# Performance work log

Hardware: AMD Instinct MI355X
Metric: run time of the kernel (lower is better)

Reference implementation:

```python
import jax, jax.numpy as jnp
import numpy as np

E, B, S, C, N, D, DFF, H, K_FREQ = 4, 16, 256, 17, 16, 32, 64, 4, 4
DH = D // H
MA_KERNELS = (4, 8, 12)


def setup_inputs() -> dict:
    key = jax.random.key(0)
    ks = jax.random.split(key, 16)
    sc = 1.0 / np.sqrt(D).astype(np.float32)
    inp = {
        "x": jax.random.normal(ks[0], (B, S, C, 1), jnp.float32),
        "original_x": jax.random.uniform(ks[1], (B, S, 2), jnp.float32),
        "start_W": jax.random.normal(ks[2], (D,), jnp.float32),
        "start_b": jnp.zeros((D,), jnp.float32),
        "Wq": jax.random.normal(ks[3], (E, D, D), jnp.float32) * sc,
        "Wk": jax.random.normal(ks[4], (E, D, D), jnp.float32) * sc,
        "Wv": jax.random.normal(ks[5], (E, D, D), jnp.float32) * sc,
        "Wo": jax.random.normal(ks[6], (E, D, D), jnp.float32) * sc,
        "ln1_g": jnp.ones((E, D), jnp.float32),
        "ln1_b": jnp.zeros((E, D), jnp.float32),
        "ln2_g": jnp.ones((E, D), jnp.float32),
        "ln2_b": jnp.zeros((E, D), jnp.float32),
        "W1": jax.random.normal(ks[7], (E, D, DFF), jnp.float32) * sc,
        "b1": jnp.zeros((E, DFF), jnp.float32),
        "W2": jax.random.normal(ks[8], (E, DFF, D), jnp.float32) * (1.0 / np.sqrt(DFF).astype(np.float32)),
        "b2": jnp.zeros((E, D), jnp.float32),
    }
    return inp


def _moving_avg(x, k):
    # x: [B,S,Ch], replicate-pad then uniform window of size k (stride 1)
    front = jnp.repeat(x[:, :1], (k - 1) // 2, axis=1)
    end = jnp.repeat(x[:, -1:], k // 2, axis=1)
    xp = jnp.concatenate([front, x, end], axis=1)  # [B, S+k-1, Ch]
    c = jnp.cumsum(xp, axis=1)
    c = jnp.concatenate([jnp.zeros_like(c[:, :1]), c], axis=1)
    return (c[:, k:] - c[:, :-k]) / jnp.asarray(k, x.dtype)


def _fourier_season(x, k):
    # ETSformer-style FourierLayer: keep top-k amplitude frequencies (excluding DC)
    s = x.shape[1]
    xf = jnp.fft.rfft(x, axis=1)            # [B,F,Ch] complex
    amp = jnp.abs(xf)
    amp = amp.at[:, 0, :].set(-jnp.inf)     # exclude DC
    topv = jax.lax.top_k(jnp.moveaxis(amp, 1, -1), k)[0]  # [B,Ch,k]
    thresh = topv[..., -1]                  # [B,Ch]
    mask = amp >= thresh[:, None, :]
    xf_m = jnp.where(mask, xf, 0)
    return jnp.fft.irfft(xf_m, n=s, axis=1).astype(x.dtype)


def _ln(z, g, b):
    m = jnp.mean(z, -1, keepdims=True)
    v = jnp.var(z, -1, keepdims=True)
    return (z - m) * jax.lax.rsqrt(v + 1e-5) * g + b


def _expert_fwd(args):
    h, wq, wk, wv, wo, g1, bg1, g2, bg2, w1, b1e, w2, b2e = args
    # h: [B,S,N,D]; pre-LN MHA over the sequence axis per (batch, node)
    z = _ln(h, g1, bg1)
    q = jnp.einsum('bsnd,de->bsne', z, wq).reshape(B, S, N, H, DH)
    k_ = jnp.einsum('bsnd,de->bsne', z, wk).reshape(B, S, N, H, DH)
    v_ = jnp.einsum('bsnd,de->bsne', z, wv).reshape(B, S, N, H, DH)
    att = jnp.einsum('bqnhd,bknhd->bnhqk', q, k_) * (1.0 / np.sqrt(DH).astype(np.float32))
    att = jax.nn.softmax(att, axis=-1)
    o = jnp.einsum('bnhqk,bknhd->bqnhd', att, v_).reshape(B, S, N, D)
    h = h + jnp.einsum('bsnd,de->bsne', o, wo)
    z2 = _ln(h, g2, bg2)
    f = jax.nn.relu(jnp.einsum('bsnd,df->bsnf', z2, w1) + b1e)
    h = h + jnp.einsum('bsnf,fd->bsnd', f, w2) + b2e
    return h


def reference(x, original_x, start_W, start_b, Wq, Wk, Wv, Wo,
              ln1_g, ln1_b, ln2_g, ln2_b, W1, b1, W2, b2):
    xc = x[:, :, :, 0]                                  # [B,S,C]
    trend = sum(_moving_avg(xc, k) for k in MA_KERNELS) / float(len(MA_KERNELS))
    season = _fourier_season(xc, K_FREQ)
    new_x = xc + season + trend                         # [B,S,C]

    scores = original_x[:, :, -1]                       # [B,S]
    bins = jnp.linspace(scores.min(), scores.max(), E + 1)
    assign = jnp.clip(jnp.searchsorted(bins, scores, side='right') - 1, 0, E - 1)  # [B,S] int

    xns = new_x[:, :, :-1]                              # [B,S,N] drop score channel
    onehot = (assign[None] == jnp.arange(E)[:, None, None])          # [E,B,S] bool
    expert_in = xns[None] * onehot[..., None].astype(xns.dtype)      # [E,B,S,N] dense zero-padded dispatch
    hidden = expert_in[..., None] * start_W + start_b                # [E,B,S,N,D] start_linear

    outs = jax.lax.map(_expert_fwd, (hidden, Wq, Wk, Wv, Wo,
                                     ln1_g, ln1_b, ln2_g, ln2_b, W1, b1, W2, b2))  # [E,B,S,N,D]
    combined = jnp.einsum('ebs,ebsnd->bsnd', onehot.astype(outs.dtype), outs)      # one-hot combine
    return combined
```

## Files before the change

### kernel.cpp

```cpp
#include <hip/hip_runtime.h>
#include <hip/hip_fp16.h>
#include <math.h>

#define BB 16
#define SS 256
#define CC 17
#define NCH 16
#define DD 32
#define DFFN 64
#define HH 4
#define DH 8
#define EE 4

#define WS_K0 16
#define WS_V0 144
#define WS_XNS 512
#define WS_SPI (WS_XNS + BB*SS*NCH)
#define WS_WT  (WS_SPI + BB*SS + 64)
#define WS_WL  (WS_WT + 6144)

#define PRE 0.51006977f

typedef __fp16 hv2 __attribute__((ext_vector_type(2)));

__device__ __forceinline__ unsigned pkh2(float a, float b) {
  hv2 r = __builtin_amdgcn_cvt_pkrtz(a, b);
  unsigned u; __builtin_memcpy(&u, &r, 4);
  return u;
}
__device__ __forceinline__ float fd2(unsigned a, unsigned b, float c) {
  hv2 av, bv;
  __builtin_memcpy(&av, &a, 4);
  __builtin_memcpy(&bv, &b, 4);
  return __builtin_amdgcn_fdot2(av, bv, c, false);
}
__device__ __forceinline__ __half2 u2h2(unsigned u) {
  __half2 h; __builtin_memcpy(&h, &u, 4); return h;
}
template<int PAT>
__device__ __forceinline__ unsigned qdpp(unsigned v) {
  return (unsigned)__builtin_amdgcn_mov_dpp((int)v, PAT, 0xF, 0xF, true);
}
template<int PAT>
__device__ __forceinline__ float qdppf(float v) {
  return __uint_as_float(qdpp<PAT>(__float_as_uint(v)));
}

__launch_bounds__(1024)
__global__ void decomp_prep_kernel(const float* __restrict__ x,
                                   const float* __restrict__ ox,
                                   const float* __restrict__ sb,
                                   const float* __restrict__ g1,
                                   const float* __restrict__ bb1,
                                   const float* __restrict__ Wq,
                                   const float* __restrict__ Wk,
                                   const float* __restrict__ Wv,
                                   const float* __restrict__ Wo,
                                   const float* __restrict__ W1,
                                   const float* __restrict__ W2,
                                   float* __restrict__ ws) {
  const int t = threadIdx.x;
  if (blockIdx.x < 256) {
    const int b = blockIdx.x / NCH;
    const int c = blockIdx.x % NCH;
    __shared__ float xs[SS];
    __shared__ float prr[1024], pii[1024];
    __shared__ float amp[129];
    __shared__ float2 YY[129];
    __shared__ float sth;
    if (t < SS) xs[t] = x[(b*SS + t)*CC + c];
    __syncthreads();
    const float TH0 = 0.024543692606170259f;
    {
      const int f = (t & 127) + 1;
      const int chunk = t >> 7;
      const int s0 = chunk * 32;
      const int ph0 = (f * s0) & 255;
      float si, cr; sincosf(TH0*(float)ph0, &si, &cr);
      float s1, c1; sincosf(TH0*(float)f, &s1, &c1);
      float xr = 0.f, xi = 0.f;
      #pragma unroll 4
      for (int k = 0; k < 32; ++k) {
        float xvv = xs[s0 + k];
        xr += xvv * cr;
        xi -= xvv * si;
        float nc = cr*c1 - si*s1;
        si = si*c1 + cr*s1;
        cr = nc;
      }
      prr[t] = xr; pii[t] = xi;
    }
    __syncthreads();
    if (t < 128) {
      float xr = 0.f, xi = 0.f;
      #pragma unroll
      for (int k2 = 0; k2 < 8; ++k2) { xr += prr[t + 128*k2]; xi += pii[t + 128*k2]; }
      prr[t] = xr; pii[t] = xi;
      amp[t+1] = sqrtf(xr*xr + xi*xi);
    }
    __syncthreads();
    if (t < 64) {
      float a0 = amp[t+1], a1 = amp[t+65];
      int i0 = t+1, i1 = t+65;
      float th = -1e30f;
      for (int r = 0; r < 4; ++r) {
        float mv = (a0 > a1) ? a0 : a1;
        int   mi = (a0 > a1) ? i0 : i1;
        for (int off = 32; off > 0; off >>= 1) {
          float ov = __shfl_xor(mv, off);
          int   oi = __shfl_xor(mi, off);
          if (ov > mv || (ov == mv && oi < mi)) { mv = ov; mi = oi; }
        }
        th = mv;
        if (mi == i0) a0 = -1e30f;
        if (mi == i1) a1 = -1e30f;
      }
      if (t == 0) sth = th;
    }
    __syncthreads();
    if (t < 128) {
      const int f = t + 1;
      float wgt = (amp[f] >= sth) ? ((f == 128) ? 1.0f : 2.0f) * (1.0f/256.0f) : 0.0f;
      YY[f] = make_float2(wgt * prr[t], wgt * pii[t]);
    }
    __syncthreads();
    {
      const int s = t & 255;
      const int fc = t >> 8;
      const int f0 = 1 + fc*32;
      const int ph0 = (s * f0) & 255;
      float si, cr; sincosf(TH0*(float)ph0, &si, &cr);
      float s1, c1; sincosf(TH0*(float)s, &s1, &c1);
      float acc = 0.f;
      #pragma unroll 4
      for (int k = 0; k < 32; ++k) {
        float2 y = YY[f0 + k];
        acc += y.x*cr - y.y*si;
        float nc = cr*c1 - si*s1;
        si = si*c1 + cr*s1;
        cr = nc;
      }
      prr[t] = acc;
    }
    __syncthreads();
    if (t < 256) {
      float season = prr[t] + prr[t+256] + prr[t+512] + prr[t+768];
      float s4 = 0.f, s8 = 0.f, s12 = 0.f;
      #pragma unroll
      for (int j = 0; j < 4; ++j)  { int p = t + j - 1; p = p < 0 ? 0 : (p > SS-1 ? SS-1 : p); s4  += xs[p]; }
      #pragma unroll
      for (int j = 0; j < 8; ++j)  { int p = t + j - 3; p = p < 0 ? 0 : (p > SS-1 ? SS-1 : p); s8  += xs[p]; }
      #pragma unroll
      for (int j = 0; j < 12; ++j) { int p = t + j - 5; p = p < 0 ? 0 : (p > SS-1 ? SS-1 : p); s12 += xs[p]; }
      float trend = (s4 * 0.25f + s8 * 0.125f + s12 * (1.0f/12.0f)) * (1.0f/3.0f);
      ws[WS_XNS + (b*SS + t)*NCH + c] = xs[t] + season + trend;
    }
  } else if (blockIdx.x < 272) {
    const int b = blockIdx.x - 256;
    __shared__ float red[32];
    __shared__ int asg[SS];
    __shared__ int cnt[EE];
    __shared__ float z0[EE*DD];
    float mn = 3e38f, mx = -3e38f;
    #pragma unroll
    for (int k = 0; k < 4; ++k) {
      float v = ox[(t + k*1024)*2 + 1];
      mn = fminf(mn, v); mx = fmaxf(mx, v);
    }
    for (int off = 32; off > 0; off >>= 1) {
      mn = fminf(mn, __shfl_xor(mn, off));
      mx = fmaxf(mx, __shfl_xor(mx, off));
    }
    if ((t & 63) == 0) { red[(t>>6)*2] = mn; red[(t>>6)*2+1] = mx; }
    __syncthreads();
    mn = red[0]; mx = red[1];
    #pragma unroll
    for (int w = 1; w < 16; ++w) { mn = fminf(mn, red[w*2]); mx = fmaxf(mx, red[w*2+1]); }
    const float step = (mx - mn) * 0.25f;
    const float e1 = mn + step, e2 = mn + 2.f*step, e3 = mn + 3.f*step;
    if (t < 256) {
      float sc = ox[(b*SS + t)*2 + 1];
      asg[t] = (sc >= e1) + (sc >= e2) + (sc >= e3);
    }
    __syncthreads();
    if (t < EE) {
      int c = 0;
      for (int s2 = 0; s2 < SS; ++s2) c += (asg[s2] == t);
      cnt[t] = c;
    }
    __syncthreads();
    int* SPw  = (int*)ws + WS_SPI;
    int* OFFw = SPw + BB*SS;
    if (t < EE) {
      int off = 0;
      for (int i = 0; i < t; ++i) off += cnt[i];
      OFFw[b*EE + t] = off;
      int kp = off;
      for (int s2 = 0; s2 < SS; ++s2) if (asg[s2] == t) SPw[b*SS + (kp++)] = s2;
    }
    if (t < 128) {
      int ee = t >> 5, d = t & 31;
      float m = 0.f;
      for (int i = 0; i < DD; ++i) m += sb[i];
      m *= (1.0f/DD);
      float var = 0.f;
      for (int i = 0; i < DD; ++i) { float df = sb[i]-m; var += df*df; }
      var *= (1.0f/DD);
      float rs = rsqrtf(var + 1e-5f);
      z0[ee*DD + d] = (sb[d]-m)*rs*g1[ee*DD+d] + bb1[ee*DD+d];
    }
    __syncthreads();
    if (b == 0 && t < 128) {
      int ee = t >> 5, d = t & 31;
      float k0 = 0.f, v0 = 0.f;
      for (int i = 0; i < DD; ++i) {
        float zz = z0[ee*DD + i];
        k0 += zz * Wk[ee*DD*DD + i*DD + d];
        v0 += zz * Wv[ee*DD*DD + i*DD + d];
      }
      ws[WS_K0 + ee*DD + d] = k0;
      ws[WS_V0 + ee*DD + d] = v0;
    }
  } else {
    unsigned* img = (unsigned*)ws + WS_WT;
    const int base_u = (blockIdx.x - 272)*4096;
    #pragma unroll
    for (int i = 0; i < 4; ++i) {
      int u = base_u + i*1024 + t;
      unsigned val;
      if (u < 6144) {
        int mat = u >> 11, r = u & 2047;
        int row = r >> 4, ip = r & 15;
        int e = row >> 5, q = row & 31;
        int d = (q & 3)*8 + (q >> 2);
        const float* Wm = (mat == 0) ? Wq : (mat == 1) ? Wk : Wv;
        const float* src = Wm + e*1024 + d;
        val = pkh2(src[ip*64], src[ip*64 + 32]);
      } else {
        int v = u - 6144;
        if (v < 2048) {
          int row = v >> 4, ip = v & 15;
          int e = row >> 5, q = row & 31;
          int d = (q & 3)*8 + (q >> 2);
          const float* src = Wo + e*1024 + d;
          val = pkh2(src[ip*64], src[ip*64 + 32]);
        } else if (v < 6144) {
          int r = v - 2048;
          int row = r >> 4, ip = r & 15;
          int e = row >> 6, q = row & 63;
          int j = (q & 3)*16 + (q >> 2);
          const float* src = W1 + e*2048 + j;
          val = pkh2(src[ip*128], src[ip*128 + 64]);
        } else {
          int r = v - 6144;
          int a = r >> 11, rr = r & 2047;
          int row = rr >> 4, ip = rr & 15;
          int e = row >> 5, q = row & 31;
          int d = (q & 3)*8 + (q >> 2);
          int jp = a*16 + ip;
          const float* src = W2 + e*2048 + d;
          val = pkh2(src[2*jp*32], src[(2*jp+1)*32]);
        }
      }
      img[u] = val;
    }
  }
}

__launch_bounds__(1024, 4)
__global__ void fused_kernel(const float* __restrict__ ws,
    const float* __restrict__ g1, const float* __restrict__ bb1,
    const float* __restrict__ sW, const float* __restrict__ sb,
    const float* __restrict__ g2, const float* __restrict__ bb2,
    const float* __restrict__ b1, const float* __restrict__ b2,
    float* __restrict__ out) {
  const int blk = blockIdx.x;
  const int n = blk & 15;
  const int b = blk >> 4;
  const int t = threadIdx.x;
  const int p = t >> 2;
  const int hh = t & 3;
  __shared__ unsigned lds[24576];
  unsigned* wT = lds + 8192;
  unsigned* wl = lds + 14336;

  {
    const unsigned* img = (const unsigned*)ws + WS_WT;
    const int wv = t >> 6;
    const int ln = t & 63;
    #pragma unroll
    for (int i = 0; i < 4; ++i) {
      const int ch = wv*4 + i;
      __builtin_amdgcn_global_load_lds(
          (const __attribute__((address_space(1))) unsigned*)(img + ch*256 + ln*4),
          (__attribute__((address_space(3))) unsigned*)(wT + ch*256 + ln*4),
          16, 0, 0);
    }
  }

  const int* SP  = (const int*)ws + WS_SPI;
  const int* OFF = SP + BB*SS;
  const int o1 = OFF[b*4+1], o2v = OFF[b*4+2], o3 = OFF[b*4+3];
  const int e = (p >= o1) + (p >= o2v) + (p >= o3);
  const int beg = (e==0) ? 0  : ((e==1) ? o1 : ((e==2) ? o2v : o3));
  const int end = (e==0) ? o1 : ((e==1) ? o2v : ((e==2) ? o3 : SS));
  const int s = SP[b*SS + p];
  const float xv = ws[WS_XNS + (b*SS + s)*NCH + n];

  float h[DD];
  #pragma unroll
  for (int d = 0; d < DD; ++d) h[d] = xv * sW[d] + sb[d];
  float m = 0.f;
  #pragma unroll
  for (int d = 0; d < DD; ++d) m += h[d];
  m *= (1.0f/DD);
  float var = 0.f;
  #pragma unroll
  for (int d = 0; d < DD; ++d) { float df = h[d]-m; var += df*df; }
  var *= (1.0f/DD);
  float rs = rsqrtf(var + 1e-5f);
  unsigned zp[16];
  #pragma unroll
  for (int ip = 0; ip < 16; ++ip) {
    float za = (h[2*ip]  -m)*rs*g1[e*DD+2*ip]   + bb1[e*DD+2*ip];
    float zb = (h[2*ip+1]-m)*rs*g1[e*DD+2*ip+1] + bb1[e*DD+2*ip+1];
    zp[ip] = pkh2(za, zb);
  }
  __syncthreads();

  float q[DH], kk[DH], vv[DH];
  #pragma unroll
  for (int dd = 0; dd < DH; ++dd) {
    const int row16 = (e*32 + dd*4 + hh)*16;
    const uint4* rq = (const uint4*)&wT[row16];
    const uint4* rk = (const uint4*)&wT[2048 + row16];
    const uint4* rv = (const uint4*)&wT[4096 + row16];
    float aq = 0.f, ak = 0.f, av = 0.f;
    #pragma unroll
    for (int g4 = 0; g4 < 4; ++g4) {
      uint4 wq4 = rq[g4], wk4 = rk[g4], wv4 = rv[g4];
      aq = fd2(zp[4*g4+0], wq4.x, aq); aq = fd2(zp[4*g4+1], wq4.y, aq);
      aq = fd2(zp[4*g4+2], wq4.z, aq); aq = fd2(zp[4*g4+3], wq4.w, aq);
      ak = fd2(zp[4*g4+0], wk4.x, ak); ak = fd2(zp[4*g4+1], wk4.y, ak);
      ak = fd2(zp[4*g4+2], wk4.z, ak); ak = fd2(zp[4*g4+3], wk4.w, ak);
      av = fd2(zp[4*g4+0], wv4.x, av); av = fd2(zp[4*g4+1], wv4.y, av);
      av = fd2(zp[4*g4+2], wv4.z, av); av = fd2(zp[4*g4+3], wv4.w, av);
    }
    q[dd] = aq * PRE; kk[dd] = ak; vv[dd] = av;
  }
  *(uint4*)&lds[p*32 + hh*8]     = make_uint4(pkh2(kk[0],kk[1]), pkh2(kk[2],kk[3]),
                                              pkh2(kk[4],kk[5]), pkh2(kk[6],kk[7]));
  *(uint4*)&lds[p*32 + hh*8 + 4] = make_uint4(pkh2(vv[0],vv[1]), pkh2(vv[2],vv[3]),
                                              pkh2(vv[4],vv[5]), pkh2(vv[6],vv[7]));
  unsigned qp2[4];
  #pragma unroll
  for (int i = 0; i < 4; ++i) qp2[i] = pkh2(q[2*i], q[2*i+1]);
  float s0 = 0.f;
  #pragma unroll
  for (int d = 0; d < DH; ++d) s0 += q[d] * ws[WS_K0 + e*DD + hh*DH + d];
  __syncthreads();

  float wsum = 0.f;
  __half2 o2[4];
  #pragma unroll
  for (int i = 0; i < 4; ++i) o2[i] = u2h2(0u);
  int jk = beg;
  for (; jk + 1 < end; jk += 2) {
    uint4 ku0 = *(const uint4*)&lds[jk*32 + hh*8];
    uint4 vu0 = *(const uint4*)&lds[jk*32 + hh*8 + 4];
    uint4 ku1 = *(const uint4*)&lds[(jk+1)*32 + hh*8];
    uint4 vu1 = *(const uint4*)&lds[(jk+1)*32 + hh*8 + 4];
    float a0 = 0.f, a1 = 0.f;
    a0 = fd2(qp2[0], ku0.x, a0); a0 = fd2(qp2[1], ku0.y, a0);
    a0 = fd2(qp2[2], ku0.z, a0); a0 = fd2(qp2[3], ku0.w, a0);
    a1 = fd2(qp2[0], ku1.x, a1); a1 = fd2(qp2[1], ku1.y, a1);
    a1 = fd2(qp2[2], ku1.z, a1); a1 = fd2(qp2[3], ku1.w, a1);
    float w0f = __builtin_amdgcn_exp2f(a0);
    float w1f = __builtin_amdgcn_exp2f(a1);
    wsum += w0f + w1f;
    __half2 w20 = u2h2(pkh2(w0f, w0f));
    __half2 w21 = u2h2(pkh2(w1f, w1f));
    o2[0] = __hfma2(w20, u2h2(vu0.x), o2[0]);
    o2[1] = __hfma2(w20, u2h2(vu0.y), o2[1]);
    o2[2] = __hfma2(w20, u2h2(vu0.z), o2[2]);
    o2[3] = __hfma2(w20, u2h2(vu0.w), o2[3]);
    o2[0] = __hfma2(w21, u2h2(vu1.x), o2[0]);
    o2[1] = __hfma2(w21, u2h2(vu1.y), o2[1]);
    o2[2] = __hfma2(w21, u2h2(vu1.z), o2[2]);
    o2[3] = __hfma2(w21, u2h2(vu1.w), o2[3]);
  }
  if (jk < end) {
    uint4 ku = *(const uint4*)&lds[jk*32 + hh*8];
    uint4 vu = *(const uint4*)&lds[jk*32 + hh*8 + 4];
    float a = 0.f;
    a = fd2(qp2[0], ku.x, a); a = fd2(qp2[1], ku.y, a);
    a = fd2(qp2[2], ku.z, a); a = fd2(qp2[3], ku.w, a);
    float wf = __builtin_amdgcn_exp2f(a);
    wsum += wf;
    __half2 w2 = u2h2(pkh2(wf, wf));
    o2[0] = __hfma2(w2, u2h2(vu.x), o2[0]);
    o2[1] = __hfma2(w2, u2h2(vu.y), o2[1]);
    o2[2] = __hfma2(w2, u2h2(vu.z), o2[2]);
    o2[3] = __hfma2(w2, u2h2(vu.w), o2[3]);
  }
  float o[DH];
  #pragma unroll
  for (int i = 0; i < 4; ++i) {
    o[2*i]   = __low2float(o2[i]);
    o[2*i+1] = __high2float(o2[i]);
  }
  const int nmis = SS - (end - beg);
  float w0 = (float)nmis * __builtin_amdgcn_exp2f(s0);
  wsum += w0;
  #pragma unroll
  for (int d = 0; d < DH; ++d) o[d] += w0 * ws[WS_V0 + e*DD + hh*DH + d];
  float inv = 1.0f / wsum;
  #pragma unroll
  for (int d = 0; d < DH; ++d) o[d] *= inv;

  unsigned oq[4];
  #pragma unroll
  for (int j = 0; j < 4; ++j) oq[j] = pkh2(o[2*j], o[2*j+1]);
  unsigned ovp[16];
  #pragma unroll
  for (int j = 0; j < 4; ++j) {
    ovp[j]    = qdpp<0x00>(oq[j]);
    ovp[4+j]  = qdpp<0x55>(oq[j]);
    ovp[8+j]  = qdpp<0xAA>(oq[j]);
    ovp[12+j] = qdpp<0xFF>(oq[j]);
  }

  float acc[DH];
  #pragma unroll
  for (int dd = 0; dd < DH; ++dd) {
    int d = hh*DH + dd;
    const uint4* row = (const uint4*)&wl[(e*32 + dd*4 + hh)*16];
    float a = xv * sW[d] + sb[d];
    #pragma unroll
    for (int g4 = 0; g4 < 4; ++g4) {
      uint4 w4 = row[g4];
      a = fd2(ovp[4*g4+0], w4.x, a); a = fd2(ovp[4*g4+1], w4.y, a);
      a = fd2(ovp[4*g4+2], w4.z, a); a = fd2(ovp[4*g4+3], w4.w, a);
    }
    acc[dd] = a;
  }

  float ssum = 0.f;
  #pragma unroll
  for (int dd = 0; dd < DH; ++dd) ssum += acc[dd];
  ssum += qdppf<0xB1>(ssum);
  ssum += qdppf<0x4E>(ssum);
  float m2 = ssum * (1.0f/DD);
  float vs = 0.f;
  #pragma unroll
  for (int dd = 0; dd < DH; ++dd) { float df = acc[dd]-m2; vs += df*df; }
  vs += qdppf<0xB1>(vs);
  vs += qdppf<0x4E>(vs);
  float rs2 = rsqrtf(vs * (1.0f/DD) + 1e-5f);
  unsigned zq[4];
  #pragma unroll
  for (int j = 0; j < 4; ++j) {
    int d = hh*DH + 2*j;
    float za = (acc[2*j]  -m2)*rs2*g2[e*DD+d]   + bb2[e*DD+d];
    float zb = (acc[2*j+1]-m2)*rs2*g2[e*DD+d+1] + bb2[e*DD+d+1];
    zq[j] = pkh2(za, zb);
  }
  unsigned zp2[16];
  #pragma unroll
  for (int j = 0; j < 4; ++j) {
    zp2[j]    = qdpp<0x00>(zq[j]);
    zp2[4+j]  = qdpp<0x55>(zq[j]);
    zp2[8+j]  = qdpp<0xAA>(zq[j]);
    zp2[12+j] = qdpp<0xFF>(zq[j]);
  }

  float f[16];
  #pragma unroll
  for (int jj = 0; jj < 16; ++jj) {
    const uint4* row = (const uint4*)&wl[2048 + (e*64 + jj*4 + hh)*16];
    float a = b1[e*DFFN + hh*16 + jj];
    #pragma unroll
    for (int g4 = 0; g4 < 4; ++g4) {
      uint4 w4 = row[g4];
      a = fd2(zp2[4*g4+0], w4.x, a); a = fd2(zp2[4*g4+1], w4.y, a);
      a = fd2(zp2[4*g4+2], w4.z, a); a = fd2(zp2[4*g4+3], w4.w, a);
    }
    f[jj] = fmaxf(a, 0.0f);
  }
  unsigned fq[8];
  #pragma unroll
  for (int j = 0; j < 8; ++j) fq[j] = pkh2(f[2*j], f[2*j+1]);
  unsigned fu[32];
  #pragma unroll
  for (int j = 0; j < 8; ++j) {
    fu[j]    = qdpp<0x00>(fq[j]);
    fu[8+j]  = qdpp<0x55>(fq[j]);
    fu[16+j] = qdpp<0xAA>(fq[j]);
    fu[24+j] = qdpp<0xFF>(fq[j]);
  }

  float acc2[DH];
  #pragma unroll
  for (int dd = 0; dd < DH; ++dd) {
    int d = hh*DH + dd;
    const int row16 = (e*32 + dd*4 + hh)*16;
    float a = acc[dd] + b2[e*DD + d];
    #pragma unroll
    for (int g4 = 0; g4 < 8; ++g4) {
      const int plane = (g4 >> 2);
      uint4 w4 = *(const uint4*)&wl[6144 + plane*2048 + row16 + 4*(g4 & 3)];
      a = fd2(fu[4*g4+0], w4.x, a); a = fd2(fu[4*g4+1], w4.y, a);
      a = fd2(fu[4*g4+2], w4.z, a); a = fd2(fu[4*g4+3], w4.w, a);
    }
    acc2[dd] = a;
  }
  float* op = out + ((size_t)((b*SS + s)*NCH + n))*DD + hh*DH;
  *(float4*)(op)     = make_float4(acc2[0], acc2[1], acc2[2], acc2[3]);
  *(float4*)(op + 4) = make_float4(acc2[4], acc2[5], acc2[6], acc2[7]);
}

extern "C" void kernel_launch(void* const* d_in, const int* in_sizes, int n_in,
                              void* d_out, int out_size, void* d_ws, size_t ws_size,
                              hipStream_t stream) {
  (void)in_sizes; (void)n_in; (void)out_size; (void)ws_size;
  const float* x   = (const float*)d_in[0];
  const float* ox  = (const float*)d_in[1];
  const float* sW  = (const float*)d_in[2];
  const float* sb  = (const float*)d_in[3];
  const float* Wq  = (const float*)d_in[4];
  const float* Wk  = (const float*)d_in[5];
  const float* Wv  = (const float*)d_in[6];
  const float* Wo  = (const float*)d_in[7];
  const float* g1  = (const float*)d_in[8];
  const float* b1n = (const float*)d_in[9];
  const float* g2  = (const float*)d_in[10];
  const float* b2n = (const float*)d_in[11];
  const float* W1  = (const float*)d_in[12];
  const float* bf1 = (const float*)d_in[13];
  const float* W2  = (const float*)d_in[14];
  const float* bf2 = (const float*)d_in[15];
  float* out = (float*)d_out;
  float* ws  = (float*)d_ws;

  decomp_prep_kernel<<<276, 1024, 0, stream>>>(x, ox, sb, g1, b1n,
                                               Wq, Wk, Wv, Wo, W1, W2, ws);
  fused_kernel<<<BB*NCH, 1024, 0, stream>>>(ws, g1, b1n, sW, sb, g2, b2n,
                                            bf1, bf2, out);
}
```

Before: 134.4 us.

## Process two query positions per thread to reuse K/V and weight loads

Each thread now handles two adjacent sorted positions, halving the block size to 512 threads. The attention loop reads each K/V row once from LDS and applies it to both queries, masking each by its expert range. Weight rows are shared when both positions map to the same expert. This roughly doubles register pressure and adds masked exp work in the attention loop, in exchange for fewer LDS loads and a smaller block.

```diff
diff --git a/kernel.cpp b/kernel.cpp
--- a/kernel.cpp
+++ b/kernel.cpp
@@ -267,7 +267,7 @@
   }
 }
 
-__launch_bounds__(1024, 4)
+__launch_bounds__(512, 2)
 __global__ void fused_kernel(const float* __restrict__ ws,
     const float* __restrict__ g1, const float* __restrict__ bb1,
     const float* __restrict__ sW, const float* __restrict__ sb,
@@ -278,8 +278,9 @@
   const int n = blk & 15;
   const int b = blk >> 4;
   const int t = threadIdx.x;
-  const int p = t >> 2;
+  const int pp = t >> 2;
   const int hh = t & 3;
+  const int p0 = pp*2, p1 = pp*2 + 1;
   __shared__ unsigned lds[24576];
   unsigned* wT = lds + 8192;
   unsigned* wl = lds + 14336;
@@ -289,8 +290,8 @@
     const int wv = t >> 6;
     const int ln = t & 63;
     #pragma unroll
-    for (int i = 0; i < 4; ++i) {
-      const int ch = wv*4 + i;
+    for (int i = 0; i < 8; ++i) {
+      const int ch = wv*8 + i;
       __builtin_amdgcn_global_load_lds(
           (const __attribute__((address_space(1))) unsigned*)(img + ch*256 + ln*4),
           (__attribute__((address_space(3))) unsigned*)(wT + ch*256 + ln*4),
@@ -301,222 +302,339 @@
   const int* SP  = (const int*)ws + WS_SPI;
   const int* OFF = SP + BB*SS;
   const int o1 = OFF[b*4+1], o2v = OFF[b*4+2], o3 = OFF[b*4+3];
-  const int e = (p >= o1) + (p >= o2v) + (p >= o3);
-  const int beg = (e==0) ? 0  : ((e==1) ? o1 : ((e==2) ? o2v : o3));
-  const int end = (e==0) ? o1 : ((e==1) ? o2v : ((e==2) ? o3 : SS));
-  const int s = SP[b*SS + p];
-  const float xv = ws[WS_XNS + (b*SS + s)*NCH + n];
-
-  float h[DD];
-  #pragma unroll
-  for (int d = 0; d < DD; ++d) h[d] = xv * sW[d] + sb[d];
-  float m = 0.f;
-  #pragma unroll
-  for (int d = 0; d < DD; ++d) m += h[d];
-  m *= (1.0f/DD);
-  float var = 0.f;
-  #pragma unroll
-  for (int d = 0; d < DD; ++d) { float df = h[d]-m; var += df*df; }
-  var *= (1.0f/DD);
-  float rs = rsqrtf(var + 1e-5f);
-  unsigned zp[16];
-  #pragma unroll
-  for (int ip = 0; ip < 16; ++ip) {
-    float za = (h[2*ip]  -m)*rs*g1[e*DD+2*ip]   + bb1[e*DD+2*ip];
-    float zb = (h[2*ip+1]-m)*rs*g1[e*DD+2*ip+1] + bb1[e*DD+2*ip+1];
-    zp[ip] = pkh2(za, zb);
+  const int e0 = (p0 >= o1) + (p0 >= o2v) + (p0 >= o3);
+  const int e1 = (p1 >= o1) + (p1 >= o2v) + (p1 >= o3);
+  const bool same_e = (e0 == e1);
+  const int beg0 = (e0==0) ? 0  : ((e0==1) ? o1 : ((e0==2) ? o2v : o3));
+  const int end0 = (e0==0) ? o1 : ((e0==1) ? o2v : ((e0==2) ? o3 : SS));
+  const int beg1 = (e1==0) ? 0  : ((e1==1) ? o1 : ((e1==2) ? o2v : o3));
+  const int end1 = (e1==0) ? o1 : ((e1==1) ? o2v : ((e1==2) ? o3 : SS));
+  const int sA = SP[b*SS + p0];
+  const int sB = SP[b*SS + p1];
+  const float xv0 = ws[WS_XNS + (b*SS + sA)*NCH + n];
+  const float xv1 = ws[WS_XNS + (b*SS + sB)*NCH + n];
+
+  unsigned zp0[16], zp1[16];
+  {
+    float h[DD];
+    #pragma unroll
+    for (int d = 0; d < DD; ++d) h[d] = xv0 * sW[d] + sb[d];
+    float m = 0.f;
+    #pragma unroll
+    for (int d = 0; d < DD; ++d) m += h[d];
+    m *= (1.0f/DD);
+    float var = 0.f;
+    #pragma unroll
+    for (int d = 0; d < DD; ++d) { float df = h[d]-m; var += df*df; }
+    float rs = rsqrtf(var*(1.0f/DD) + 1e-5f);
+    #pragma unroll
+    for (int ip = 0; ip < 16; ++ip) {
+      float za = (h[2*ip]  -m)*rs*g1[e0*DD+2*ip]   + bb1[e0*DD+2*ip];
+      float zb = (h[2*ip+1]-m)*rs*g1[e0*DD+2*ip+1] + bb1[e0*DD+2*ip+1];
+      zp0[ip] = pkh2(za, zb);
+    }
+  }
+  {
+    float h[DD];
+    #pragma unroll
+    for (int d = 0; d < DD; ++d) h[d] = xv1 * sW[d] + sb[d];
+    float m = 0.f;
+    #pragma unroll
+    for (int d = 0; d < DD; ++d) m += h[d];
+    m *= (1.0f/DD);
+    float var = 0.f;
+    #pragma unroll
+    for (int d = 0; d < DD; ++d) { float df = h[d]-m; var += df*df; }
+    float rs = rsqrtf(var*(1.0f/DD) + 1e-5f);
+    #pragma unroll
+    for (int ip = 0; ip < 16; ++ip) {
+      float za = (h[2*ip]  -m)*rs*g1[e1*DD+2*ip]   + bb1[e1*DD+2*ip];
+      float zb = (h[2*ip+1]-m)*rs*g1[e1*DD+2*ip+1] + bb1[e1*DD+2*ip+1];
+      zp1[ip] = pkh2(za, zb);
+    }
   }
   __syncthreads();
 
-  float q[DH], kk[DH], vv[DH];
+  float q0[DH], q1[DH], kk0[DH], kk1[DH], vv0[DH], vv1[DH];
   #pragma unroll
   for (int dd = 0; dd < DH; ++dd) {
-    const int row16 = (e*32 + dd*4 + hh)*16;
-    const uint4* rq = (const uint4*)&wT[row16];
-    const uint4* rk = (const uint4*)&wT[2048 + row16];
-    const uint4* rv = (const uint4*)&wT[4096 + row16];
-    float aq = 0.f, ak = 0.f, av = 0.f;
+    const int r0 = (e0*32 + dd*4 + hh)*16;
+    const uint4* rq = (const uint4*)&wT[r0];
+    const uint4* rk = (const uint4*)&wT[2048 + r0];
+    const uint4* rv = (const uint4*)&wT[4096 + r0];
+    float aq0=0.f, ak0=0.f, av0=0.f, aq1=0.f, ak1=0.f, av1=0.f;
     #pragma unroll
     for (int g4 = 0; g4 < 4; ++g4) {
       uint4 wq4 = rq[g4], wk4 = rk[g4], wv4 = rv[g4];
-      aq = fd2(zp[4*g4+0], wq4.x, aq); aq = fd2(zp[4*g4+1], wq4.y, aq);
-      aq = fd2(zp[4*g4+2], wq4.z, aq); aq = fd2(zp[4*g4+3], wq4.w, aq);
-      ak = fd2(zp[4*g4+0], wk4.x, ak); ak = fd2(zp[4*g4+1], wk4.y, ak);
-      ak = fd2(zp[4*g4+2], wk4.z, ak); ak = fd2(zp[4*g4+3], wk4.w, ak);
-      av = fd2(zp[4*g4+0], wv4.x, av); av = fd2(zp[4*g4+1], wv4.y, av);
-      av = fd2(zp[4*g4+2], wv4.z, av); av = fd2(zp[4*g4+3], wv4.w, av);
-    }
-    q[dd] = aq * PRE; kk[dd] = ak; vv[dd] = av;
-  }
-  *(uint4*)&lds[p*32 + hh*8]     = make_uint4(pkh2(kk[0],kk[1]), pkh2(kk[2],kk[3]),
-                                              pkh2(kk[4],kk[5]), pkh2(kk[6],kk[7]));
-  *(uint4*)&lds[p*32 + hh*8 + 4] = make_uint4(pkh2(vv[0],vv[1]), pkh2(vv[2],vv[3]),
-                                              pkh2(vv[4],vv[5]), pkh2(vv[6],vv[7]));
-  unsigned qp2[4];
-  #pragma unroll
-  for (int i = 0; i < 4; ++i) qp2[i] = pkh2(q[2*i], q[2*i+1]);
-  float s0 = 0.f;
-  #pragma unroll
-  for (int d = 0; d < DH; ++d) s0 += q[d] * ws[WS_K0 + e*DD + hh*DH + d];
+      aq0 = fd2(zp0[4*g4+0], wq4.x, aq0); aq0 = fd2(zp0[4*g4+1], wq4.y, aq0);
+      aq0 = fd2(zp0[4*g4+2], wq4.z, aq0); aq0 = fd2(zp0[4*g4+3], wq4.w, aq0);
+      ak0 = fd2(zp0[4*g4+0], wk4.x, ak0); ak0 = fd2(zp0[4*g4+1], wk4.y, ak0);
+      ak0 = fd2(zp0[4*g4+2], wk4.z, ak0); ak0 = fd2(zp0[4*g4+3], wk4.w, ak0);
+      av0 = fd2(zp0[4*g4+0], wv4.x, av0); av0 = fd2(zp0[4*g4+1], wv4.y, av0);
+      av0 = fd2(zp0[4*g4+2], wv4.z, av0); av0 = fd2(zp0[4*g4+3], wv4.w, av0);
+      if (same_e) {
+        aq1 = fd2(zp1[4*g4+0], wq4.x, aq1); aq1 = fd2(zp1[4*g4+1], wq4.y, aq1);
+        aq1 = fd2(zp1[4*g4+2], wq4.z, aq1); aq1 = fd2(zp1[4*g4+3], wq4.w, aq1);
+        ak1 = fd2(zp1[4*g4+0], wk4.x, ak1); ak1 = fd2(zp1[4*g4+1], wk4.y, ak1);
+        ak1 = fd2(zp1[4*g4+2], wk4.z, ak1); ak1 = fd2(zp1[4*g4+3], wk4.w, ak1);
+        av1 = fd2(zp1[4*g4+0], wv4.x, av1); av1 = fd2(zp1[4*g4+1], wv4.y, av1);
+        av1 = fd2(zp1[4*g4+2], wv4.z, av1); av1 = fd2(zp1[4*g4+3], wv4.w, av1);
+      }
+    }
+    if (!same_e) {
+      const int r1 = (e1*32 + dd*4 + hh)*16;
+      const uint4* rq1p = (const uint4*)&wT[r1];
+      const uint4* rk1p = (const uint4*)&wT[2048 + r1];
+      const uint4* rv1p = (const uint4*)&wT[4096 + r1];
+      #pragma unroll
+      for (int g4 = 0; g4 < 4; ++g4) {
+        uint4 wq4 = rq1p[g4], wk4 = rk1p[g4], wv4 = rv1p[g4];
+        aq1 = fd2(zp1[4*g4+0], wq4.x, aq1); aq1 = fd2(zp1[4*g4+1], wq4.y, aq1);
+        aq1 = fd2(zp1[4*g4+2], wq4.z, aq1); aq1 = fd2(zp1[4*g4+3], wq4.w, aq1);
+        ak1 = fd2(zp1[4*g4+0], wk4.x, ak1); ak1 = fd2(zp1[4*g4+1], wk4.y, ak1);
+        ak1 = fd2(zp1[4*g4+2], wk4.z, ak1); ak1 = fd2(zp1[4*g4+3], wk4.w, ak1);
+        av1 = fd2(zp1[4*g4+0], wv4.x, av1); av1 = fd2(zp1[4*g4+1], wv4.y, av1);
+        av1 = fd2(zp1[4*g4+2], wv4.z, av1); av1 = fd2(zp1[4*g4+3], wv4.w, av1);
+      }
+    }
+    q0[dd] = aq0 * PRE; kk0[dd] = ak0; vv0[dd] = av0;
+    q1[dd] = aq1 * PRE; kk1[dd] = ak1; vv1[dd] = av1;
+  }
+  *(uint4*)&lds[p0*32 + hh*8]     = make_uint4(pkh2(kk0[0],kk0[1]), pkh2(kk0[2],kk0[3]),
+                                               pkh2(kk0[4],kk0[5]), pkh2(kk0[6],kk0[7]));
+  *(uint4*)&lds[p0*32 + hh*8 + 4] = make_uint4(pkh2(vv0[0],vv0[1]), pkh2(vv0[2],vv0[3]),
+                                               pkh2(vv0[4],vv0[5]), pkh2(vv0[6],vv0[7]));
+  *(uint4*)&lds[p1*32 + hh*8]     = make_uint4(pkh2(kk1[0],kk1[1]), pkh2(kk1[2],kk1[3]),
+                                               pkh2(kk1[4],kk1[5]), pkh2(kk1[6],kk1[7]));
+  *(uint4*)&lds[p1*32 + hh*8 + 4] = make_uint4(pkh2(vv1[0],vv1[1]), pkh2(vv1[2],vv1[3]),
+                                               pkh2(vv1[4],vv1[5]), pkh2(vv1[6],vv1[7]));
+  unsigned qp20[4], qp21[4];
+  #pragma unroll
+  for (int i = 0; i < 4; ++i) {
+    qp20[i] = pkh2(q0[2*i], q0[2*i+1]);
+    qp21[i] = pkh2(q1[2*i], q1[2*i+1]);
+  }
+  float sc0 = 0.f, sc1 = 0.f;
+  #pragma unroll
+  for (int d = 0; d < DH; ++d) {
+    sc0 += q0[d] * ws[WS_K0 + e0*DD + hh*DH + d];
+    sc1 += q1[d] * ws[WS_K0 + e1*DD + hh*DH + d];
+  }
   __syncthreads();
 
-  float wsum = 0.f;
-  __half2 o2[4];
-  #pragma unroll
-  for (int i = 0; i < 4; ++i) o2[i] = u2h2(0u);
-  int jk = beg;
-  for (; jk + 1 < end; jk += 2) {
-    uint4 ku0 = *(const uint4*)&lds[jk*32 + hh*8];
-    uint4 vu0 = *(const uint4*)&lds[jk*32 + hh*8 + 4];
-    uint4 ku1 = *(const uint4*)&lds[(jk+1)*32 + hh*8];
-    uint4 vu1 = *(const uint4*)&lds[(jk+1)*32 + hh*8 + 4];
+  float wsum0 = 0.f, wsum1 = 0.f;
+  __half2 oa[4], ob[4];
+  #pragma unroll
+  for (int i = 0; i < 4; ++i) { oa[i] = u2h2(0u); ob[i] = u2h2(0u); }
+  for (int j = beg0; j < end1; ++j) {
+    uint4 ku = *(const uint4*)&lds[j*32 + hh*8];
+    uint4 vu = *(const uint4*)&lds[j*32 + hh*8 + 4];
     float a0 = 0.f, a1 = 0.f;
-    a0 = fd2(qp2[0], ku0.x, a0); a0 = fd2(qp2[1], ku0.y, a0);
-    a0 = fd2(qp2[2], ku0.z, a0); a0 = fd2(qp2[3], ku0.w, a0);
-    a1 = fd2(qp2[0], ku1.x, a1); a1 = fd2(qp2[1], ku1.y, a1);
-    a1 = fd2(qp2[2], ku1.z, a1); a1 = fd2(qp2[3], ku1.w, a1);
-    float w0f = __builtin_amdgcn_exp2f(a0);
-    float w1f = __builtin_amdgcn_exp2f(a1);
-    wsum += w0f + w1f;
-    __half2 w20 = u2h2(pkh2(w0f, w0f));
-    __half2 w21 = u2h2(pkh2(w1f, w1f));
-    o2[0] = __hfma2(w20, u2h2(vu0.x), o2[0]);
-    o2[1] = __hfma2(w20, u2h2(vu0.y), o2[1]);
-    o2[2] = __hfma2(w20, u2h2(vu0.z), o2[2]);
-    o2[3] = __hfma2(w20, u2h2(vu0.w), o2[3]);
-    o2[0] = __hfma2(w21, u2h2(vu1.x), o2[0]);
-    o2[1] = __hfma2(w21, u2h2(vu1.y), o2[1]);
-    o2[2] = __hfma2(w21, u2h2(vu1.z), o2[2]);
-    o2[3] = __hfma2(w21, u2h2(vu1.w), o2[3]);
-  }
-  if (jk < end) {
-    uint4 ku = *(const uint4*)&lds[jk*32 + hh*8];
-    uint4 vu = *(const uint4*)&lds[jk*32 + hh*8 + 4];
-    float a = 0.f;
-    a = fd2(qp2[0], ku.x, a); a = fd2(qp2[1], ku.y, a);
-    a = fd2(qp2[2], ku.z, a); a = fd2(qp2[3], ku.w, a);
-    float wf = __builtin_amdgcn_exp2f(a);
-    wsum += wf;
-    __half2 w2 = u2h2(pkh2(wf, wf));
-    o2[0] = __hfma2(w2, u2h2(vu.x), o2[0]);
-    o2[1] = __hfma2(w2, u2h2(vu.y), o2[1]);
-    o2[2] = __hfma2(w2, u2h2(vu.z), o2[2]);
-    o2[3] = __hfma2(w2, u2h2(vu.w), o2[3]);
-  }
-  float o[DH];
+    a0 = fd2(qp20[0], ku.x, a0); a0 = fd2(qp20[1], ku.y, a0);
+    a0 = fd2(qp20[2], ku.z, a0); a0 = fd2(qp20[3], ku.w, a0);
+    a1 = fd2(qp21[0], ku.x, a1); a1 = fd2(qp21[1], ku.y, a1);
+    a1 = fd2(qp21[2], ku.z, a1); a1 = fd2(qp21[3], ku.w, a1);
+    float w0k = (j < end0)  ? __builtin_amdgcn_exp2f(a0) : 0.f;
+    float w1k = (j >= beg1) ? __builtin_amdgcn_exp2f(a1) : 0.f;
+    wsum0 += w0k; wsum1 += w1k;
+    __half2 w20 = u2h2(pkh2(w0k, w0k));
+    __half2 w21 = u2h2(pkh2(w1k, w1k));
+    oa[0] = __hfma2(w20, u2h2(vu.x), oa[0]);
+    oa[1] = __hfma2(w20, u2h2(vu.y), oa[1]);
+    oa[2] = __hfma2(w20, u2h2(vu.z), oa[2]);
+    oa[3] = __hfma2(w20, u2h2(vu.w), oa[3]);
+    ob[0] = __hfma2(w21, u2h2(vu.x), ob[0]);
+    ob[1] = __hfma2(w21, u2h2(vu.y), ob[1]);
+    ob[2] = __hfma2(w21, u2h2(vu.z), ob[2]);
+    ob[3] = __hfma2(w21, u2h2(vu.w), ob[3]);
+  }
+  float o0[DH], o1v[DH];
   #pragma unroll
   for (int i = 0; i < 4; ++i) {
-    o[2*i]   = __low2float(o2[i]);
-    o[2*i+1] = __high2float(o2[i]);
-  }
-  const int nmis = SS - (end - beg);
-  float w0 = (float)nmis * __builtin_amdgcn_exp2f(s0);
-  wsum += w0;
-  #pragma unroll
-  for (int d = 0; d < DH; ++d) o[d] += w0 * ws[WS_V0 + e*DD + hh*DH + d];
-  float inv = 1.0f / wsum;
-  #pragma unroll
-  for (int d = 0; d < DH; ++d) o[d] *= inv;
-
-  unsigned oq[4];
-  #pragma unroll
-  for (int j = 0; j < 4; ++j) oq[j] = pkh2(o[2*j], o[2*j+1]);
-  unsigned ovp[16];
-  #pragma unroll
-  for (int j = 0; j < 4; ++j) {
-    ovp[j]    = qdpp<0x00>(oq[j]);
-    ovp[4+j]  = qdpp<0x55>(oq[j]);
-    ovp[8+j]  = qdpp<0xAA>(oq[j]);
-    ovp[12+j] = qdpp<0xFF>(oq[j]);
-  }
-
-  float acc[DH];
+    o0[2*i]   = __low2float(oa[i]);  o0[2*i+1]  = __high2float(oa[i]);
+    o1v[2*i]  = __low2float(ob[i]);  o1v[2*i+1] = __high2float(ob[i]);
+  }
+  {
+    const int nm0 = SS - (end0 - beg0);
+    const int nm1 = SS - (end1 - beg1);
+    float w00 = (float)nm0 * __builtin_amdgcn_exp2f(sc0);
+    float w01 = (float)nm1 * __builtin_amdgcn_exp2f(sc1);
+    wsum0 += w00; wsum1 += w01;
+    #pragma unroll
+    for (int d = 0; d < DH; ++d) {
+      o0[d]  += w00 * ws[WS_V0 + e0*DD + hh*DH + d];
+      o1v[d] += w01 * ws[WS_V0 + e1*DD + hh*DH + d];
+    }
+    float i0 = 1.0f / wsum0, i1 = 1.0f / wsum1;
+    #pragma unroll
+    for (int d = 0; d < DH; ++d) { o0[d] *= i0; o1v[d] *= i1; }
+  }
+
+  unsigned ovp0[16], ovp1[16];
+  {
+    unsigned oqa[4], oqb[4];
+    #pragma unroll
+    for (int j = 0; j < 4; ++j) {
+      oqa[j] = pkh2(o0[2*j], o0[2*j+1]);
+      oqb[j] = pkh2(o1v[2*j], o1v[2*j+1]);
+    }
+    #pragma unroll
+    for (int j = 0; j < 4; ++j) {
+      ovp0[j]    = qdpp<0x00>(oqa[j]);  ovp1[j]    = qdpp<0x00>(oqb[j]);
+      ovp0[4+j]  = qdpp<0x55>(oqa[j]);  ovp1[4+j]  = qdpp<0x55>(oqb[j]);
+      ovp0[8+j]  = qdpp<0xAA>(oqa[j]);  ovp1[8+j]  = qdpp<0xAA>(oqb[j]);
+      ovp0[12+j] = qdpp<0xFF>(oqa[j]);  ovp1[12+j] = qdpp<0xFF>(oqb[j]);
+    }
+  }
+
+  float acc0[DH], acc1[DH];
   #pragma unroll
   for (int dd = 0; dd < DH; ++dd) {
-    int d = hh*DH + dd;
-    const uint4* row = (const uint4*)&wl[(e*32 + dd*4 + hh)*16];
-    float a = xv * sW[d] + sb[d];
+    const int d = hh*DH + dd;
+    const uint4* row0 = (const uint4*)&wl[(e0*32 + dd*4 + hh)*16];
+    float a0 = xv0 * sW[d] + sb[d];
+    float a1 = xv1 * sW[d] + sb[d];
     #pragma unroll
     for (int g4 = 0; g4 < 4; ++g4) {
-      uint4 w4 = row[g4];
-      a = fd2(ovp[4*g4+0], w4.x, a); a = fd2(ovp[4*g4+1], w4.y, a);
-      a = fd2(ovp[4*g4+2], w4.z, a); a = fd2(ovp[4*g4+3], w4.w, a);
-    }
-    acc[dd] = a;
-  }
-
-  float ssum = 0.f;
-  #pragma unroll
-  for (int dd = 0; dd < DH; ++dd) ssum += acc[dd];
-  ssum += qdppf<0xB1>(ssum);
-  ssum += qdppf<0x4E>(ssum);
-  float m2 = ssum * (1.0f/DD);
-  float vs = 0.f;
-  #pragma unroll
-  for (int dd = 0; dd < DH; ++dd) { float df = acc[dd]-m2; vs += df*df; }
-  vs += qdppf<0xB1>(vs);
-  vs += qdppf<0x4E>(vs);
-  float rs2 = rsqrtf(vs * (1.0f/DD) + 1e-5f);
-  unsigned zq[4];
-  #pragma unroll
-  for (int j = 0; j < 4; ++j) {
-    int d = hh*DH + 2*j;
-    float za = (acc[2*j]  -m2)*rs2*g2[e*DD+d]   + bb2[e*DD+d];
-    float zb = (acc[2*j+1]-m2)*rs2*g2[e*DD+d+1] + bb2[e*DD+d+1];
-    zq[j] = pkh2(za, zb);
-  }
-  unsigned zp2[16];
-  #pragma unroll
-  for (int j = 0; j < 4; ++j) {
-    zp2[j]    = qdpp<0x00>(zq[j]);
-    zp2[4+j]  = qdpp<0x55>(zq[j]);
-    zp2[8+j]  = qdpp<0xAA>(zq[j]);
-    zp2[12+j] = qdpp<0xFF>(zq[j]);
-  }
-
-  float f[16];
+      uint4 w4 = row0[g4];
+      a0 = fd2(ovp0[4*g4+0], w4.x, a0); a0 = fd2(ovp0[4*g4+1], w4.y, a0);
+      a0 = fd2(ovp0[4*g4+2], w4.z, a0); a0 = fd2(ovp0[4*g4+3], w4.w, a0);
+      if (same_e) {
+        a1 = fd2(ovp1[4*g4+0], w4.x, a1); a1 = fd2(ovp1[4*g4+1], w4.y, a1);
+        a1 = fd2(ovp1[4*g4+2], w4.z, a1); a1 = fd2(ovp1[4*g4+3], w4.w, a1);
+      }
+    }
+    if (!same_e) {
+      const uint4* row1 = (const uint4*)&wl[(e1*32 + dd*4 + hh)*16];
+      #pragma unroll
+      for (int g4 = 0; g4 < 4; ++g4) {
+        uint4 w4 = row1[g4];
+        a1 = fd2(ovp1[4*g4+0], w4.x, a1); a1 = fd2(ovp1[4*g4+1], w4.y, a1);
+        a1 = fd2(ovp1[4*g4+2], w4.z, a1); a1 = fd2(ovp1[4*g4+3], w4.w, a1);
+      }
+    }
+    acc0[dd] = a0; acc1[dd] = a1;
+  }
+
+  unsigned zq20[16], zq21[16];
+  {
+    float s0s = 0.f, s1s = 0.f;
+    #pragma unroll
+    for (int dd = 0; dd < DH; ++dd) { s0s += acc0[dd]; s1s += acc1[dd]; }
+    s0s += qdppf<0xB1>(s0s); s0s += qdppf<0x4E>(s0s);
+    s1s += qdppf<0xB1>(s1s); s1s += qdppf<0x4E>(s1s);
+    float m0 = s0s * (1.0f/DD), m1 = s1s * (1.0f/DD);
+    float v0 = 0.f, v1 = 0.f;
+    #pragma unroll
+    for (int dd = 0; dd < DH; ++dd) {
+      float d0 = acc0[dd]-m0; v0 += d0*d0;
+      float d1 = acc1[dd]-m1; v1 += d1*d1;
+    }
+    v0 += qdppf<0xB1>(v0); v0 += qdppf<0x4E>(v0);
+    v1 += qdppf<0xB1>(v1); v1 += qdppf<0x4E>(v1);
+    float r0 = rsqrtf(v0*(1.0f/DD) + 1e-5f);
+    float r1 = rsqrtf(v1*(1.0f/DD) + 1e-5f);
+    unsigned za0[4], za1[4];
+    #pragma unroll
+    for (int j = 0; j < 4; ++j) {
+      int d = hh*DH + 2*j;
+      float x0 = (acc0[2*j]  -m0)*r0*g2[e0*DD+d]   + bb2[e0*DD+d];
+      float y0 = (acc0[2*j+1]-m0)*r0*g2[e0*DD+d+1] + bb2[e0*DD+d+1];
+      float x1 = (acc1[2*j]  -m1)*r1*g2[e1*DD+d]   + bb2[e1*DD+d];
+      float y1 = (acc1[2*j+1]-m1)*r1*g2[e1*DD+d+1] + bb2[e1*DD+d+1];
+      za0[j] = pkh2(x0, y0);
+      za1[j] = pkh2(x1, y1);
+    }
+    #pragma unroll
+    for (int j = 0; j < 4; ++j) {
+      zq20[j]    = qdpp<0x00>(za0[j]);  zq21[j]    = qdpp<0x00>(za1[j]);
+      zq20[4+j]  = qdpp<0x55>(za0[j]);  zq21[4+j]  = qdpp<0x55>(za1[j]);
+      zq20[8+j]  = qdpp<0xAA>(za0[j]);  zq21[8+j]  = qdpp<0xAA>(za1[j]);
+      zq20[12+j] = qdpp<0xFF>(za0[j]);  zq21[12+j] = qdpp<0xFF>(za1[j]);
+    }
+  }
+
+  float f0[16], f1[16];
   #pragma unroll
   for (int jj = 0; jj < 16; ++jj) {
-    const uint4* row = (const uint4*)&wl[2048 + (e*64 + jj*4 + hh)*16];
-    float a = b1[e*DFFN + hh*16 + jj];
+    const uint4* row0 = (const uint4*)&wl[2048 + (e0*64 + jj*4 + hh)*16];
+    float a0 = b1[e0*DFFN + hh*16 + jj];
+    float a1 = b1[e1*DFFN + hh*16 + jj];
     #pragma unroll
     for (int g4 = 0; g4 < 4; ++g4) {
-      uint4 w4 = row[g4];
-      a = fd2(zp2[4*g4+0], w4.x, a); a = fd2(zp2[4*g4+1], w4.y, a);
-      a = fd2(zp2[4*g4+2], w4.z, a); a = fd2(zp2[4*g4+3], w4.w, a);
-    }
-    f[jj] = fmaxf(a, 0.0f);
-  }
-  unsigned fq[8];
-  #pragma unroll
-  for (int j = 0; j < 8; ++j) fq[j] = pkh2(f[2*j], f[2*j+1]);
-  unsigned fu[32];
-  #pragma unroll
-  for (int j = 0; j < 8; ++j) {
-    fu[j]    = qdpp<0x00>(fq[j]);
-    fu[8+j]  = qdpp<0x55>(fq[j]);
-    fu[16+j] = qdpp<0xAA>(fq[j]);
-    fu[24+j] = qdpp<0xFF>(fq[j]);
-  }
-
-  float acc2[DH];
+      uint4 w4 = row0[g4];
+      a0 = fd2(zq20[4*g4+0], w4.x, a0); a0 = fd2(zq20[4*g4+1], w4.y, a0);
+      a0 = fd2(zq20[4*g4+2], w4.z, a0); a0 = fd2(zq20[4*g4+3], w4.w, a0);
+      if (same_e) {
+        a1 = fd2(zq21[4*g4+0], w4.x, a1); a1 = fd2(zq21[4*g4+1], w4.y, a1);
+        a1 = fd2(zq21[4*g4+2], w4.z, a1); a1 = fd2(zq21[4*g4+3], w4.w, a1);
+      }
+    }
+    if (!same_e) {
+      const uint4* row1 = (const uint4*)&wl[2048 + (e1*64 + jj*4 + hh)*16];
+      #pragma unroll
+      for (int g4 = 0; g4 < 4; ++g4) {
+        uint4 w4 = row1[g4];
+        a1 = fd2(zq21[4*g4+0], w4.x, a1); a1 = fd2(zq21[4*g4+1], w4.y, a1);
+        a1 = fd2(zq21[4*g4+2], w4.z, a1); a1 = fd2(zq21[4*g4+3], w4.w, a1);
+      }
+    }
+    f0[jj] = fmaxf(a0, 0.0f);
+    f1[jj] = fmaxf(a1, 0.0f);
+  }
+  unsigned fu0[32], fu1[32];
+  {
+    unsigned fq0[8], fq1[8];
+    #pragma unroll
+    for (int j = 0; j < 8; ++j) {
+      fq0[j] = pkh2(f0[2*j], f0[2*j+1]);
+      fq1[j] = pkh2(f1[2*j], f1[2*j+1]);
+    }
+    #pragma unroll
+    for (int j = 0; j < 8; ++j) {
+      fu0[j]    = qdpp<0x00>(fq0[j]);  fu1[j]    = qdpp<0x00>(fq1[j]);
+      fu0[8+j]  = qdpp<0x55>(fq0[j]);  fu1[8+j]  = qdpp<0x55>(fq1[j]);
+      fu0[16+j] = qdpp<0xAA>(fq0[j]);  fu1[16+j] = qdpp<0xAA>(fq1[j]);
+      fu0[24+j] = qdpp<0xFF>(fq0[j]);  fu1[24+j] = qdpp<0xFF>(fq1[j]);
+    }
+  }
+
+  float acc20[DH], acc21[DH];
   #pragma unroll
   for (int dd = 0; dd < DH; ++dd) {
-    int d = hh*DH + dd;
-    const int row16 = (e*32 + dd*4 + hh)*16;
-    float a = acc[dd] + b2[e*DD + d];
+    const int d = hh*DH + dd;
+    const int r160 = (e0*32 + dd*4 + hh)*16;
+    float a0 = acc0[dd] + b2[e0*DD + d];
+    float a1 = acc1[dd] + b2[e1*DD + d];
     #pragma unroll
     for (int g4 = 0; g4 < 8; ++g4) {
       const int plane = (g4 >> 2);
-      uint4 w4 = *(const uint4*)&wl[6144 + plane*2048 + row16 + 4*(g4 & 3)];
-      a = fd2(fu[4*g4+0], w4.x, a); a = fd2(fu[4*g4+1], w4.y, a);
-      a = fd2(fu[4*g4+2], w4.z, a); a = fd2(fu[4*g4+3], w4.w, a);
-    }
-    acc2[dd] = a;
-  }
-  float* op = out + ((size_t)((b*SS + s)*NCH + n))*DD + hh*DH;
-  *(float4*)(op)     = make_float4(acc2[0], acc2[1], acc2[2], acc2[3]);
-  *(float4*)(op + 4) = make_float4(acc2[4], acc2[5], acc2[6], acc2[7]);
+      uint4 w4 = *(const uint4*)&wl[6144 + plane*2048 + r160 + 4*(g4 & 3)];
+      a0 = fd2(fu0[4*g4+0], w4.x, a0); a0 = fd2(fu0[4*g4+1], w4.y, a0);
+      a0 = fd2(fu0[4*g4+2], w4.z, a0); a0 = fd2(fu0[4*g4+3], w4.w, a0);
+      if (same_e) {
+        a1 = fd2(fu1[4*g4+0], w4.x, a1); a1 = fd2(fu1[4*g4+1], w4.y, a1);
+        a1 = fd2(fu1[4*g4+2], w4.z, a1); a1 = fd2(fu1[4*g4+3], w4.w, a1);
+      }
+    }
+    if (!same_e) {
+      const int r161 = (e1*32 + dd*4 + hh)*16;
+      #pragma unroll
+      for (int g4 = 0; g4 < 8; ++g4) {
+        const int plane = (g4 >> 2);
+        uint4 w4 = *(const uint4*)&wl[6144 + plane*2048 + r161 + 4*(g4 & 3)];
+        a1 = fd2(fu1[4*g4+0], w4.x, a1); a1 = fd2(fu1[4*g4+1], w4.y, a1);
+        a1 = fd2(fu1[4*g4+2], w4.z, a1); a1 = fd2(fu1[4*g4+3], w4.w, a1);
+      }
+    }
+    acc20[dd] = a0; acc21[dd] = a1;
+  }
+  float* op0 = out + ((size_t)((b*SS + sA)*NCH + n))*DD + hh*DH;
+  *(float4*)(op0)     = make_float4(acc20[0], acc20[1], acc20[2], acc20[3]);
+  *(float4*)(op0 + 4) = make_float4(acc20[4], acc20[5], acc20[6], acc20[7]);
+  float* op1 = out + ((size_t)((b*SS + sB)*NCH + n))*DD + hh*DH;
+  *(float4*)(op1)     = make_float4(acc21[0], acc21[1], acc21[2], acc21[3]);
+  *(float4*)(op1 + 4) = make_float4(acc21[4], acc21[5], acc21[6], acc21[7]);
 }
 
 extern "C" void kernel_launch(void* const* d_in, const int* in_sizes, int n_in,
@@ -544,6 +662,6 @@
 
   decomp_prep_kernel<<<276, 1024, 0, stream>>>(x, ox, sb, g1, b1n,
                                                Wq, Wk, Wv, Wo, W1, W2, ws);
-  fused_kernel<<<BB*NCH, 1024, 0, stream>>>(ws, g1, b1n, sW, sb, g2, b2n,
-                                            bf1, bf2, out);
-}
+  fused_kernel<<<BB*NCH, 512, 0, stream>>>(ws, g1, b1n, sW, sb, g2, b2n,
+                                           bf1, bf2, out);
+}
```

New measurement: 238.1 us. +77.2%, slower.
